# Kernel tuning notes

Measured on AMD Instinct MI355X. Metric: run time of the kernel, lower is better.

Reference implementation:

```python
import math
import jax, jax.numpy as jnp
import numpy as np

N_EMBD = 1024
N_HEAD = 16
EPS = 1e-5


def get_alibi_slopes(n_head):
    def pow2_slopes(n):
        start = 2 ** (-2 ** (-(math.log2(n) - 3)))
        return [start * start ** i for i in range(n)]
    if math.log2(n_head).is_integer():
        slopes = pow2_slopes(n_head)
    else:
        c = 2 ** math.floor(math.log2(n_head))
        slopes = pow2_slopes(c)
        extra = pow2_slopes(2 * c)[0::2]
        slopes.extend(extra[: n_head - c])
    return jnp.asarray(slopes, dtype=jnp.float32)


def layernorm(x, w, b):
    mu = jnp.mean(x, axis=-1, keepdims=True)
    var = jnp.var(x, axis=-1, keepdims=True)
    return (x - mu) * jax.lax.rsqrt(var + EPS) * w + b


def setup_inputs() -> dict:
    key = jax.random.key(0)
    ks = jax.random.split(key, 8)
    C = N_EMBD
    B, T = 2, 2048
    s = 0.02
    return {
        "x": jax.random.normal(ks[0], (B, T, C), dtype=jnp.float32),
        "ln1_w": jnp.ones((C,), jnp.float32),
        "ln1_b": jnp.zeros((C,), jnp.float32),
        "w_qkv": jax.random.normal(ks[1], (C, 3 * C), dtype=jnp.float32) * s,
        "b_qkv": jnp.zeros((3 * C,), jnp.float32),
        "w_proj": jax.random.normal(ks[2], (C, C), dtype=jnp.float32) * s,
        "b_proj": jnp.zeros((C,), jnp.float32),
        "ln2_w": jnp.ones((C,), jnp.float32),
        "ln2_b": jnp.zeros((C,), jnp.float32),
        "w_fc": jax.random.normal(ks[3], (C, 4 * C), dtype=jnp.float32) * s,
        "b_fc": jnp.zeros((4 * C,), jnp.float32),
        "w_fc2": jax.random.normal(ks[4], (4 * C, C), dtype=jnp.float32) * s,
        "b_fc2": jnp.zeros((C,), jnp.float32),
    }


def reference(x, ln1_w, ln1_b, w_qkv, b_qkv, w_proj, b_proj,
              ln2_w, ln2_b, w_fc, b_fc, w_fc2, b_fc2):
    B, T, C = x.shape
    H = N_HEAD
    D = C // H

    # --- attention with ALiBi ---
    h = layernorm(x, ln1_w, ln1_b)
    qkv = h @ w_qkv + b_qkv                       # [B,T,3C]
    q, k, v = jnp.split(qkv, 3, axis=-1)
    q = q.reshape(B, T, H, D).transpose(0, 2, 1, 3)  # [B,H,T,D]
    k = k.reshape(B, T, H, D).transpose(0, 2, 1, 3)
    v = v.reshape(B, T, H, D).transpose(0, 2, 1, 3)

    att = jnp.einsum('bhqd,bhkd->bhqk', q, k) * (1.0 / math.sqrt(D))

    pos = jnp.arange(T, dtype=jnp.float32)
    distances = pos[:, None] - pos[None, :]        # [T,T], i-j
    slopes = get_alibi_slopes(H)[:, None, None]     # [H,1,1]
    bias = slopes * distances[None, :, :]           # [H,T,T]
    causal = jnp.triu(jnp.ones((T, T), dtype=bool), k=1)
    bias = jnp.where(causal[None, :, :], -jnp.inf, bias)

    att = jax.nn.softmax(att + bias[None], axis=-1)
    y = jnp.einsum('bhqk,bhkd->bhqd', att, v)
    y = y.transpose(0, 2, 1, 3).reshape(B, T, C)
    x = x + y @ w_proj + b_proj

    # --- MLP ---
    h = layernorm(x, ln2_w, ln2_b)
    h = jax.nn.gelu(h @ w_fc + b_fc, approximate=False)
    x = x + h @ w_fc2 + b_fc2
    return x
```

## Files before the change

### kernel.cpp

```cpp
#include <hip/hip_runtime.h>
#include <hip/hip_bf16.h>
#include <math.h>

#define N_EMBD 1024
#define N_HEADC 16
#define HEAD_D 64

typedef __attribute__((ext_vector_type(8))) short short8;
typedef __attribute__((ext_vector_type(4))) float floatx4;

__device__ __forceinline__ ushort f2b(float f) {
    __hip_bfloat16 h = __float2bfloat16(f);
    return *reinterpret_cast<ushort*>(&h);
}

__device__ __forceinline__ void async_cp16(const void* gsrc, void* ldst) {
    __builtin_amdgcn_global_load_lds(
        (const __attribute__((address_space(1))) void*)gsrc,
        (__attribute__((address_space(3))) void*)ldst, 16, 0, 0);
}

__device__ __forceinline__ int xcd_swizzle(int bid, int nwg) {
    const int q = nwg >> 3, r = nwg & 7;
    const int xcd = bid & 7, loc = bid >> 3;
    return (xcd < r ? xcd * (q + 1) : r * (q + 1) + (xcd - r) * q) + loc;
}

template <int CTRL>
__device__ __forceinline__ float dppf(float x) {
    int r = __builtin_amdgcn_update_dpp(0, __builtin_bit_cast(int, x),
                                        CTRL, 0xF, 0xF, true);
    return __builtin_bit_cast(float, r);
}
__device__ __forceinline__ float redmax16(float x) {
    x = fmaxf(x, dppf<0xB1>(x));
    x = fmaxf(x, dppf<0x4E>(x));
    x = fmaxf(x, dppf<0x141>(x));
    x = fmaxf(x, dppf<0x140>(x));
    return x;
}
__device__ __forceinline__ float redsum16(float x) {
    x += dppf<0xB1>(x);
    x += dppf<0x4E>(x);
    x += dppf<0x141>(x);
    x += dppf<0x140>(x);
    return x;
}

__global__ __launch_bounds__(256) void ln_kernel(const float* __restrict__ x,
                                                 const float* __restrict__ w,
                                                 const float* __restrict__ b,
                                                 ushort* __restrict__ out) {
    const int row = blockIdx.x;
    const int t = threadIdx.x;
    const float4 v = reinterpret_cast<const float4*>(x + (size_t)row * N_EMBD)[t];
    float s  = v.x + v.y + v.z + v.w;
    float ss = v.x * v.x + v.y * v.y + v.z * v.z + v.w * v.w;
    for (int o = 32; o > 0; o >>= 1) {
        s  += __shfl_down(s, o);
        ss += __shfl_down(ss, o);
    }
    __shared__ float as_[4], ass_[4];
    const int wid = t >> 6, lane = t & 63;
    if (lane == 0) { as_[wid] = s; ass_[wid] = ss; }
    __syncthreads();
    const float ts  = as_[0] + as_[1] + as_[2] + as_[3];
    const float tss = ass_[0] + ass_[1] + ass_[2] + ass_[3];
    const float mu  = ts * (1.f / N_EMBD);
    const float var = tss * (1.f / N_EMBD) - mu * mu;
    const float inv = rsqrtf(var + 1e-5f);
    const float4 wv = reinterpret_cast<const float4*>(w)[t];
    const float4 bv = reinterpret_cast<const float4*>(b)[t];
    ushort4 o;
    o.x = f2b((v.x - mu) * inv * wv.x + bv.x);
    o.y = f2b((v.y - mu) * inv * wv.y + bv.y);
    o.z = f2b((v.z - mu) * inv * wv.z + bv.z);
    o.w = f2b((v.w - mu) * inv * wv.w + bv.w);
    reinterpret_cast<ushort4*>(out + (size_t)row * N_EMBD)[t] = o;
}

__global__ void convtrans_kernel(const float* __restrict__ W,
                                 ushort* __restrict__ Wt, int K, int N) {
    __shared__ float tile[32][33];
    const int tid = threadIdx.x;
    const int r = tid >> 3;
    const int c4 = (tid & 7) * 4;
    const int bx = blockIdx.x, by = blockIdx.y;

    float4 v = *(const float4*)&W[((size_t)(by * 32 + r)) * N + bx * 32 + c4];
    tile[r][c4 + 0] = v.x; tile[r][c4 + 1] = v.y;
    tile[r][c4 + 2] = v.z; tile[r][c4 + 3] = v.w;
    __syncthreads();

    ushort4 u;
    u.x = f2b(tile[c4 + 0][r]); u.y = f2b(tile[c4 + 1][r]);
    u.z = f2b(tile[c4 + 2][r]); u.w = f2b(tile[c4 + 3][r]);
    *(ushort4*)&Wt[((size_t)(bx * 32 + r)) * K + by * 32 + c4] = u;
}

__device__ __forceinline__ void gemm_stage(
        const ushort* __restrict__ A, const ushort* __restrict__ Bt,
        ushort* As, ushort* Bs,
        int m0, int n0, int K, int k0, int w, int lane) {
#pragma unroll
    for (int l = 0; l < 2; l++) {
        const int cbase = w * 128 + l * 64;
        const int c = cbase + lane;
        const int row = c >> 2, kc8 = (c & 3) * 8;
        async_cp16(A  + (size_t)(m0 + row) * K + k0 + kc8, &As[cbase * 8]);
        async_cp16(Bt + (size_t)(n0 + row) * K + k0 + kc8, &Bs[cbase * 8]);
    }
}

__device__ __forceinline__ void gemm_compute(
        const ushort* As, const ushort* Bs, floatx4 (*acc)[4],
        int wm, int wn, int quad, int l16) {
    short8 a[4], bf[4];
#pragma unroll
    for (int i = 0; i < 4; i++)
        a[i] = *(const short8*)&As[(wm * 64 + i * 16 + l16) * 32 + quad * 8];
#pragma unroll
    for (int j = 0; j < 4; j++)
        bf[j] = *(const short8*)&Bs[(wn * 64 + j * 16 + l16) * 32 + quad * 8];
#pragma unroll
    for (int i = 0; i < 4; i++)
#pragma unroll
        for (int j = 0; j < 4; j++)
            acc[i][j] = __builtin_amdgcn_mfma_f32_16x16x32_bf16(
                a[i], bf[j], acc[i][j], 0, 0, 0);
}

__global__ __launch_bounds__(256) void gemm_bf16_kernel(
        const ushort* __restrict__ A,
        const ushort* __restrict__ Bt,
        const float* __restrict__ bias,
        const float* __restrict__ residual,
        float* __restrict__ out32,
        ushort* __restrict__ out16,
        int M, int N, int K, int do_gelu) {
    __shared__ ushort As[2][128 * 32];
    __shared__ ushort Bs[2][128 * 32];

    const int tid  = threadIdx.x;
    const int w    = tid >> 6;
    const int lane = tid & 63;
    const int quad = lane >> 4;
    const int l16  = lane & 15;
    const int wm   = w >> 1;
    const int wn   = w & 1;

    int bid = blockIdx.y * gridDim.x + blockIdx.x;
    bid = xcd_swizzle(bid, gridDim.x * gridDim.y);
    const int bx = bid % gridDim.x;
    const int by = bid / gridDim.x;
    const int m0 = by * 128;
    const int n0 = bx * 128;

    const int kchunk = K / gridDim.z;
    const int kbeg   = blockIdx.z * kchunk;
    if (gridDim.z > 1)
        out32 += (size_t)blockIdx.z * M * N;

    floatx4 acc[4][4];
#pragma unroll
    for (int i = 0; i < 4; i++)
#pragma unroll
        for (int j = 0; j < 4; j++) acc[i][j] = (floatx4){0.f, 0.f, 0.f, 0.f};

    const int nt = kchunk >> 5;

    gemm_stage(A, Bt, As[0], Bs[0], m0, n0, K, kbeg, w, lane);
    __syncthreads();

    for (int t = 0; t < nt; t += 2) {
        gemm_stage(A, Bt, As[1], Bs[1], m0, n0, K, kbeg + ((t + 1) << 5), w, lane);
        gemm_compute(As[0], Bs[0], acc, wm, wn, quad, l16);
        __syncthreads();
        if (t + 2 < nt)
            gemm_stage(A, Bt, As[0], Bs[0], m0, n0, K, kbeg + ((t + 2) << 5), w, lane);
        gemm_compute(As[1], Bs[1], acc, wm, wn, quad, l16);
        __syncthreads();
    }

#pragma unroll
    for (int i = 0; i < 4; i++) {
#pragma unroll
        for (int j = 0; j < 4; j++) {
            const int nn = n0 + wn * 64 + j * 16 + l16;
            const float bv = bias ? bias[nn] : 0.f;
#pragma unroll
            for (int r = 0; r < 4; r++) {
                const int mm = m0 + wm * 64 + i * 16 + quad * 4 + r;
                float v = acc[i][j][r] + bv;
                if (do_gelu) v = 0.5f * v * (1.f + erff(v * 0.70710678118654752f));
                if (residual) v += residual[(size_t)mm * N + nn];
                if (out32) out32[(size_t)mm * N + nn] = v;
                if (out16) out16[(size_t)mm * N + nn] = f2b(v);
            }
        }
    }
}

__global__ __launch_bounds__(256) void combine_kernel(
        const float* __restrict__ p0, const float* __restrict__ p1,
        const float* __restrict__ bias, float* __restrict__ out) {
    const int i = blockIdx.x * 256 + threadIdx.x;
    const float4 a = ((const float4*)p0)[i];
    const float4 c = ((const float4*)p1)[i];
    const float4 bb = ((const float4*)bias)[i & 255];
    float4 o = ((float4*)out)[i];
    o.x += a.x + c.x + bb.x;
    o.y += a.y + c.y + bb.y;
    o.z += a.z + c.z + bb.z;
    o.w += a.w + c.w + bb.w;
    ((float4*)out)[i] = o;
}

#define AT_PAD 72
#define LOG2E 1.4426950408889634f

__device__ __forceinline__ void attn_tile_step(
        short8 aq0, short8 aq1,
        ushort (*__restrict__ Ks)[AT_PAD],
        ushort (*__restrict__ Vt)[AT_PAD],
        ushort (*__restrict__ Ps)[AT_PAD],
        float* m_r, float* l_r, floatx4* acc,
        int q0, int kt, bool domask,
        float qs2, float slope2, const float* skb,
        int w, int quad, int l16) {
    floatx4 sfrag[4];
#pragma unroll
    for (int kb = 0; kb < 4; kb++) {
        const int kcol = kb * 16 + l16;
        short8 bk0 = *(const short8*)&Ks[kcol][quad * 8];
        short8 bk1 = *(const short8*)&Ks[kcol][32 + quad * 8];
        floatx4 s = (floatx4){0.f, 0.f, 0.f, 0.f};
        s = __builtin_amdgcn_mfma_f32_16x16x32_bf16(aq0, bk0, s, 0, 0, 0);
        s = __builtin_amdgcn_mfma_f32_16x16x32_bf16(aq1, bk1, s, 0, 0, 0);
        sfrag[kb] = s;
    }

    const int psw = ((w * 4 + quad) & 7) << 3;
    int pcol[4];
#pragma unroll
    for (int kb = 0; kb < 4; kb++) pcol[kb] = (kb * 16 + l16) ^ psw;

    const float ktb = (float)(kt * 64);
#pragma unroll
    for (int r = 0; r < 4; r++) {
        const int q = q0 + w * 16 + quad * 4 + r;
        const float rowc = slope2 * ((float)q - ktb);
        float sv[4];
        float rm = -INFINITY;
#pragma unroll
        for (int kb = 0; kb < 4; kb++) {
            float s = fmaf(sfrag[kb][r], qs2, rowc) - skb[kb];
            if (domask) {
                const int k = kt * 64 + kb * 16 + l16;
                s = (k <= q) ? s : -INFINITY;
            }
            sv[kb] = s;
            rm = fmaxf(rm, s);
        }
        rm = redmax16(rm);
        if (rm > m_r[r]) {
            const float corr = exp2f(m_r[r] - rm);
            m_r[r] = rm;
            l_r[r] *= corr;
#pragma unroll
            for (int db = 0; db < 4; db++) acc[db][r] *= corr;
        }
        float rs = 0.f;
#pragma unroll
        for (int kb = 0; kb < 4; kb++) {
            const float pv = exp2f(sv[kb] - m_r[r]);
            rs += pv;
            Ps[w * 16 + quad * 4 + r][pcol[kb]] = f2b(pv);
        }
        rs = redsum16(rs);
        l_r[r] += rs;
    }

    const int prw = ((w * 4 + (l16 >> 2)) & 7) << 3;
    short8 ap0 = *(const short8*)&Ps[w * 16 + l16][(quad * 8) ^ prw];
    short8 ap1 = *(const short8*)&Ps[w * 16 + l16][(32 + quad * 8) ^ prw];
#pragma unroll
    for (int db = 0; db < 4; db++) {
        const int dv = db * 16 + l16;
        const int svw = ((db * 4 + (l16 >> 2)) & 7) << 3;
        short8 bv0 = *(const short8*)&Vt[dv][(quad * 8) ^ svw];
        short8 bv1 = *(const short8*)&Vt[dv][(32 + quad * 8) ^ svw];
        acc[db] = __builtin_amdgcn_mfma_f32_16x16x32_bf16(ap0, bv0, acc[db], 0, 0, 0);
        acc[db] = __builtin_amdgcn_mfma_f32_16x16x32_bf16(ap1, bv1, acc[db], 0, 0, 0);
    }
}

__global__ __launch_bounds__(256) void attn_mfma_kernel(
        const ushort* __restrict__ qkv, ushort* __restrict__ y,
        float* __restrict__ opart, float* __restrict__ mpart,
        float* __restrict__ lpart, int B, int T) {
    const int C3 = 3 * N_EMBD;

    const int lin = xcd_swizzle(blockIdx.x, gridDim.x);
    const int bh = lin / 48;
    const int s  = lin % 48;
    int qt, cc, ktb_i, kte;
    bool split;
    if (s < 32) {
        split = true;
        qt = 31 - (s >> 1);
        cc = s & 1;
        const int hc = (qt + 2) >> 1;
        ktb_i = cc ? hc : 0;
        kte   = cc ? qt : hc - 1;
    } else {
        split = false;
        qt = 47 - s;
        cc = 0;
        ktb_i = 0;
        kte = qt;
    }
    const int b = bh >> 4, h = bh & 15;

    const int tid  = threadIdx.x;
    const int lane = tid & 63;
    const int w    = tid >> 6;
    const int quad = lane >> 4;
    const int l16  = lane & 15;

    __shared__ ushort QPs[64][AT_PAD];
    __shared__ ushort Ks[64][AT_PAD];
    __shared__ ushort Vt[64][AT_PAD];

    const float slope  = exp2f(-0.5f * (float)(h + 1));
    const float slope2 = slope * LOG2E;
    const float qs2    = 0.125f * LOG2E;
    float skb[4];
#pragma unroll
    for (int kb = 0; kb < 4; kb++) skb[kb] = slope2 * (float)(kb * 16 + l16);

    const int q0 = qt * 64;
    const size_t hb = (size_t)b * T * C3 + (size_t)h * HEAD_D;

    int srow[4], sd0[4], svr[4];
#pragma unroll
    for (int i = 0; i < 4; i++) {
        const int idx = tid + i * 256;
        srow[i] = idx >> 4;
        sd0[i]  = (idx & 15) * 4;
        svr[i]  = srow[i] ^ ((idx & 7) << 3);
    }

#pragma unroll
    for (int i = 0; i < 4; i++) {
        *(ushort4*)&QPs[srow[i]][sd0[i]] =
            *(const ushort4*)&qkv[hb + (size_t)(q0 + srow[i]) * C3 + sd0[i]];
    }
    __syncthreads();

    const int mrow = w * 16 + l16;
    short8 aq0 = *(const short8*)&QPs[mrow][quad * 8];
    short8 aq1 = *(const short8*)&QPs[mrow][32 + quad * 8];

    float m_r[4], l_r[4];
    floatx4 acc[4];
#pragma unroll
    for (int r = 0; r < 4; r++) {
        m_r[r] = -INFINITY; l_r[r] = 0.f;
        acc[r] = (floatx4){0.f, 0.f, 0.f, 0.f};
    }

#pragma unroll
    for (int i = 0; i < 4; i++) {
        const size_t src = hb + (size_t)(ktb_i * 64 + srow[i]) * C3 + sd0[i];
        *(ushort4*)&Ks[srow[i]][sd0[i]] = *(const ushort4*)&qkv[src + N_EMBD];
        ushort4 vv = *(const ushort4*)&qkv[src + 2 * N_EMBD];
        Vt[sd0[i] + 0][svr[i]] = vv.x;
        Vt[sd0[i] + 1][svr[i]] = vv.y;
        Vt[sd0[i] + 2][svr[i]] = vv.z;
        Vt[sd0[i] + 3][svr[i]] = vv.w;
    }
    __syncthreads();

    for (int kt = ktb_i; kt <= kte; kt++) {
        ushort4 kreg[4], vreg[4];
        const bool pf = (kt < kte);
        if (pf) {
#pragma unroll
            for (int i = 0; i < 4; i++) {
                const size_t src =
                    hb + (size_t)((kt + 1) * 64 + srow[i]) * C3 + sd0[i];
                kreg[i] = *(const ushort4*)&qkv[src + N_EMBD];
                vreg[i] = *(const ushort4*)&qkv[src + 2 * N_EMBD];
            }
        }

        attn_tile_step(aq0, aq1, Ks, Vt, QPs, m_r, l_r, acc,
                       q0, kt, kt == qt, qs2, slope2, skb, w, quad, l16);
        __syncthreads();

        if (pf) {
#pragma unroll
            for (int i = 0; i < 4; i++) {
                *(ushort4*)&Ks[srow[i]][sd0[i]] = kreg[i];
                Vt[sd0[i] + 0][svr[i]] = vreg[i].x;
                Vt[sd0[i] + 1][svr[i]] = vreg[i].y;
                Vt[sd0[i] + 2][svr[i]] = vreg[i].z;
                Vt[sd0[i] + 3][svr[i]] = vreg[i].w;
            }
        }
        __syncthreads();
    }

    if (!split) {
#pragma unroll
        for (int r = 0; r < 4; r++) {
            const int qa = q0 + w * 16 + quad * 4 + r;
            const float ia = 1.f / l_r[r];
#pragma unroll
            for (int db = 0; db < 4; db++) {
                y[((size_t)b * T + qa) * N_EMBD + h * HEAD_D + db * 16 + l16] =
                    f2b(acc[db][r] * ia);
            }
        }
    } else {
        const int pidx = (bh * 16 + (qt - 16)) * 2 + cc;
#pragma unroll
        for (int r = 0; r < 4; r++) {
            const int row = w * 16 + quad * 4 + r;
#pragma unroll
            for (int db = 0; db < 4; db++) {
                opart[((size_t)pidx * 64 + row) * 64 + db * 16 + l16] =
                    acc[db][r];
            }
            if (l16 == 0) {
                mpart[pidx * 64 + row] = m_r[r];
                lpart[pidx * 64 + row] = l_r[r];
            }
        }
    }
}

__global__ __launch_bounds__(256) void attn_combine_kernel(
        const float* __restrict__ opart, const float* __restrict__ mpart,
        const float* __restrict__ lpart, ushort* __restrict__ y, int T) {
    const int x  = blockIdx.x;
    const int bh = x >> 4;
    const int qt = 16 + (x & 15);
    const int b  = bh >> 4, h = bh & 15;
    const int t  = threadIdx.x;
    const int row = t >> 2;
    const int dq  = (t & 3) << 4;
    const int p0 = x * 2, p1 = p0 + 1;

    const float m0 = mpart[p0 * 64 + row], m1 = mpart[p1 * 64 + row];
    const float l0 = lpart[p0 * 64 + row], l1 = lpart[p1 * 64 + row];
    const float M  = fmaxf(m0, m1);
    const float w0 = exp2f(m0 - M), w1 = exp2f(m1 - M);
    const float inv = 1.f / (l0 * w0 + l1 * w1);

    const float* o0 = &opart[((size_t)p0 * 64 + row) * 64 + dq];
    const float* o1 = &opart[((size_t)p1 * 64 + row) * 64 + dq];
    ushort* yr = &y[((size_t)b * T + qt * 64 + row) * N_EMBD + h * HEAD_D + dq];
#pragma unroll
    for (int j = 0; j < 16; j += 4) {
        const float4 a = *(const float4*)&o0[j];
        const float4 c = *(const float4*)&o1[j];
        yr[j + 0] = f2b((a.x * w0 + c.x * w1) * inv);
        yr[j + 1] = f2b((a.y * w0 + c.y * w1) * inv);
        yr[j + 2] = f2b((a.z * w0 + c.z * w1) * inv);
        yr[j + 3] = f2b((a.w * w0 + c.w * w1) * inv);
    }
}

extern "C" void kernel_launch(void* const* d_in, const int* in_sizes, int n_in,
                              void* d_out, int out_size, void* d_ws, size_t ws_size,
                              hipStream_t stream) {
    const int B = 2, T = 2048, C = N_EMBD;
    const int M = B * T;

    const float* x      = (const float*)d_in[0];
    const float* ln1_w  = (const float*)d_in[1];
    const float* ln1_b  = (const float*)d_in[2];
    const float* w_qkv  = (const float*)d_in[3];
    const float* b_qkv  = (const float*)d_in[4];
    const float* w_proj = (const float*)d_in[5];
    const float* b_proj = (const float*)d_in[6];
    const float* ln2_w  = (const float*)d_in[7];
    const float* ln2_b  = (const float*)d_in[8];
    const float* w_fc   = (const float*)d_in[9];
    const float* b_fc   = (const float*)d_in[10];
    const float* w_fc2  = (const float*)d_in[11];
    const float* b_fc2  = (const float*)d_in[12];
    float* out = (float*)d_out;

    char* ws = (char*)d_ws;
    size_t off = 0;
    ushort* wt_qkv  = (ushort*)(ws + off); off += (size_t)3 * C * C * 2;
    ushort* wt_proj = (ushort*)(ws + off); off += (size_t)C * C * 2;
    ushort* wt_fc   = (ushort*)(ws + off); off += (size_t)4 * C * C * 2;
    ushort* wt_fc2  = (ushort*)(ws + off); off += (size_t)4 * C * C * 2;
    ushort* h16     = (ushort*)(ws + off); off += (size_t)M * C * 2;
    ushort* qkv16   = (ushort*)(ws + off); off += (size_t)M * 3 * C * 2;
    ushort* y16     = (ushort*)(ws + off); off += (size_t)M * C * 2;
    ushort* fc16    = (ushort*)(ws + off); off += (size_t)M * 4 * C * 2;

    convtrans_kernel<<<dim3(3 * C / 32, C / 32), 256, 0, stream>>>(w_qkv, wt_qkv, C, 3 * C);
    convtrans_kernel<<<dim3(C / 32, C / 32), 256, 0, stream>>>(w_proj, wt_proj, C, C);
    convtrans_kernel<<<dim3(4 * C / 32, C / 32), 256, 0, stream>>>(w_fc, wt_fc, C, 4 * C);
    convtrans_kernel<<<dim3(C / 32, 4 * C / 32), 256, 0, stream>>>(w_fc2, wt_fc2, 4 * C, C);

    ln_kernel<<<M, 256, 0, stream>>>(x, ln1_w, ln1_b, h16);

    gemm_bf16_kernel<<<dim3(3 * C / 128, M / 128), 256, 0, stream>>>(
        h16, wt_qkv, b_qkv, nullptr, nullptr, qkv16, M, 3 * C, C, 0);

    float* aop = (float*)fc16;
    float* amp = aop + (size_t)1024 * 64 * 64;
    float* alp = amp + (size_t)1024 * 64;
    attn_mfma_kernel<<<32 * 48, 256, 0, stream>>>(
        qkv16, y16, aop, amp, alp, B, T);
    attn_combine_kernel<<<512, 256, 0, stream>>>(aop, amp, alp, y16, T);

    gemm_bf16_kernel<<<dim3(C / 128, M / 128), 256, 0, stream>>>(
        y16, wt_proj, b_proj, x, out, nullptr, M, C, C, 0);

    ln_kernel<<<M, 256, 0, stream>>>(out, ln2_w, ln2_b, h16);

    gemm_bf16_kernel<<<dim3(4 * C / 128, M / 128), 256, 0, stream>>>(
        h16, wt_fc, b_fc, nullptr, nullptr, fc16, M, 4 * C, C, 1);

    float* part = (float*)h16;
    gemm_bf16_kernel<<<dim3(C / 128, M / 128, 2), 256, 0, stream>>>(
        fc16, wt_fc2, nullptr, nullptr, part, nullptr, M, C, 4 * C, 0);
    combine_kernel<<<(M * C) / (256 * 4), 256, 0, stream>>>(
        part, part + (size_t)M * C, b_fc2, out);
}
```

Before: 437.0 us.

## Compute transposed S tile so each lane owns one query row in attention

Swaps the MFMA operands in the QK^T step so the score fragment is S^T: each lane now holds 16 scores for a single query row instead of 4 rows. Row max and sum then need only two cross-lane shuffles per tile instead of a DPP reduction per row, and each lane keeps one m/l scalar. P is written to LDS as packed ushort4 without the XOR swizzle. The cost is extra shuffles to broadcast the rescale factors to accumulator rows, and possible LDS bank conflicts on the unswizzled P writes and reads.

```diff
diff --git a/kernel.cpp b/kernel.cpp
--- a/kernel.cpp
+++ b/kernel.cpp
@@ -24,27 +24,6 @@
     const int q = nwg >> 3, r = nwg & 7;
     const int xcd = bid & 7, loc = bid >> 3;
     return (xcd < r ? xcd * (q + 1) : r * (q + 1) + (xcd - r) * q) + loc;
-}
-
-template <int CTRL>
-__device__ __forceinline__ float dppf(float x) {
-    int r = __builtin_amdgcn_update_dpp(0, __builtin_bit_cast(int, x),
-                                        CTRL, 0xF, 0xF, true);
-    return __builtin_bit_cast(float, r);
-}
-__device__ __forceinline__ float redmax16(float x) {
-    x = fmaxf(x, dppf<0xB1>(x));
-    x = fmaxf(x, dppf<0x4E>(x));
-    x = fmaxf(x, dppf<0x141>(x));
-    x = fmaxf(x, dppf<0x140>(x));
-    return x;
-}
-__device__ __forceinline__ float redsum16(float x) {
-    x += dppf<0xB1>(x);
-    x += dppf<0x4E>(x);
-    x += dppf<0x141>(x);
-    x += dppf<0x140>(x);
-    return x;
 }
 
 __global__ __launch_bounds__(256) void ln_kernel(const float* __restrict__ x,
@@ -224,66 +203,75 @@
         ushort (*__restrict__ Ks)[AT_PAD],
         ushort (*__restrict__ Vt)[AT_PAD],
         ushort (*__restrict__ Ps)[AT_PAD],
-        float* m_r, float* l_r, floatx4* acc,
-        int q0, int kt, bool domask,
-        float qs2, float slope2, const float* skb,
-        int w, int quad, int l16) {
+        float& m_row, float& l_row, floatx4* acc,
+        int qrow, int kt, bool domask,
+        float qs2, float alibi_q, float skb16, const float* skq4,
+        int w, int quad, int l16, int lane) {
     floatx4 sfrag[4];
 #pragma unroll
     for (int kb = 0; kb < 4; kb++) {
-        const int kcol = kb * 16 + l16;
-        short8 bk0 = *(const short8*)&Ks[kcol][quad * 8];
-        short8 bk1 = *(const short8*)&Ks[kcol][32 + quad * 8];
+        const int krow = kb * 16 + l16;
+        short8 ak0 = *(const short8*)&Ks[krow][quad * 8];
+        short8 ak1 = *(const short8*)&Ks[krow][32 + quad * 8];
         floatx4 s = (floatx4){0.f, 0.f, 0.f, 0.f};
-        s = __builtin_amdgcn_mfma_f32_16x16x32_bf16(aq0, bk0, s, 0, 0, 0);
-        s = __builtin_amdgcn_mfma_f32_16x16x32_bf16(aq1, bk1, s, 0, 0, 0);
+        s = __builtin_amdgcn_mfma_f32_16x16x32_bf16(ak0, aq0, s, 0, 0, 0);
+        s = __builtin_amdgcn_mfma_f32_16x16x32_bf16(ak1, aq1, s, 0, 0, 0);
         sfrag[kb] = s;
     }
 
-    const int psw = ((w * 4 + quad) & 7) << 3;
-    int pcol[4];
-#pragma unroll
-    for (int kb = 0; kb < 4; kb++) pcol[kb] = (kb * 16 + l16) ^ psw;
-
-    const float ktb = (float)(kt * 64);
-#pragma unroll
-    for (int r = 0; r < 4; r++) {
-        const int q = q0 + w * 16 + quad * 4 + r;
-        const float rowc = slope2 * ((float)q - ktb);
-        float sv[4];
-        float rm = -INFINITY;
-#pragma unroll
-        for (int kb = 0; kb < 4; kb++) {
-            float s = fmaf(sfrag[kb][r], qs2, rowc) - skb[kb];
+    const float rowc = alibi_q - skb16 * (float)(kt * 4);
+    float sv[4][4];
+    float rm = -INFINITY;
+#pragma unroll
+    for (int kb = 0; kb < 4; kb++) {
+        const float rck = rowc - skb16 * (float)kb;
+#pragma unroll
+        for (int r = 0; r < 4; r++) {
+            float s = fmaf(sfrag[kb][r], qs2, rck - skq4[r]);
             if (domask) {
-                const int k = kt * 64 + kb * 16 + l16;
-                s = (k <= q) ? s : -INFINITY;
+                const int k = kt * 64 + kb * 16 + quad * 4 + r;
+                s = (k <= qrow) ? s : -INFINITY;
             }
-            sv[kb] = s;
+            sv[kb][r] = s;
             rm = fmaxf(rm, s);
         }
-        rm = redmax16(rm);
-        if (rm > m_r[r]) {
-            const float corr = exp2f(m_r[r] - rm);
-            m_r[r] = rm;
-            l_r[r] *= corr;
-#pragma unroll
-            for (int db = 0; db < 4; db++) acc[db][r] *= corr;
-        }
-        float rs = 0.f;
-#pragma unroll
-        for (int kb = 0; kb < 4; kb++) {
-            const float pv = exp2f(sv[kb] - m_r[r]);
-            rs += pv;
-            Ps[w * 16 + quad * 4 + r][pcol[kb]] = f2b(pv);
-        }
-        rs = redsum16(rs);
-        l_r[r] += rs;
-    }
-
-    const int prw = ((w * 4 + (l16 >> 2)) & 7) << 3;
-    short8 ap0 = *(const short8*)&Ps[w * 16 + l16][(quad * 8) ^ prw];
-    short8 ap1 = *(const short8*)&Ps[w * 16 + l16][(32 + quad * 8) ^ prw];
+    }
+    rm = fmaxf(rm, __shfl_xor(rm, 16));
+    rm = fmaxf(rm, __shfl_xor(rm, 32));
+
+    if (__any(rm > m_row)) {
+        const float mn = fmaxf(rm, m_row);
+        const float corr = exp2f(m_row - mn);
+        m_row = mn;
+        l_row *= corr;
+        float cr[4];
+#pragma unroll
+        for (int r = 0; r < 4; r++)
+            cr[r] = __shfl(corr, (lane & 48) + quad * 4 + r);
+#pragma unroll
+        for (int db = 0; db < 4; db++)
+#pragma unroll
+            for (int r = 0; r < 4; r++) acc[db][r] *= cr[r];
+    }
+
+    float rs = 0.f;
+#pragma unroll
+    for (int kb = 0; kb < 4; kb++) {
+        const float p0 = exp2f(sv[kb][0] - m_row);
+        const float p1 = exp2f(sv[kb][1] - m_row);
+        const float p2 = exp2f(sv[kb][2] - m_row);
+        const float p3 = exp2f(sv[kb][3] - m_row);
+        rs += (p0 + p1) + (p2 + p3);
+        ushort4 pw;
+        pw.x = f2b(p0); pw.y = f2b(p1); pw.z = f2b(p2); pw.w = f2b(p3);
+        *(ushort4*)&Ps[w * 16 + l16][kb * 16 + quad * 4] = pw;
+    }
+    rs += __shfl_xor(rs, 16);
+    rs += __shfl_xor(rs, 32);
+    l_row += rs;
+
+    short8 ap0 = *(const short8*)&Ps[w * 16 + l16][quad * 8];
+    short8 ap1 = *(const short8*)&Ps[w * 16 + l16][32 + quad * 8];
 #pragma unroll
     for (int db = 0; db < 4; db++) {
         const int dv = db * 16 + l16;
@@ -335,11 +323,15 @@
     const float slope  = exp2f(-0.5f * (float)(h + 1));
     const float slope2 = slope * LOG2E;
     const float qs2    = 0.125f * LOG2E;
-    float skb[4];
-#pragma unroll
-    for (int kb = 0; kb < 4; kb++) skb[kb] = slope2 * (float)(kb * 16 + l16);
 
     const int q0 = qt * 64;
+    const int qrow = q0 + w * 16 + l16;
+    const float alibi_q = slope2 * (float)qrow;
+    const float skb16   = slope2 * 16.f;
+    float skq4[4];
+#pragma unroll
+    for (int r = 0; r < 4; r++) skq4[r] = slope2 * (float)(quad * 4 + r);
+
     const size_t hb = (size_t)b * T * C3 + (size_t)h * HEAD_D;
 
     int srow[4], sd0[4], svr[4];
@@ -362,13 +354,10 @@
     short8 aq0 = *(const short8*)&QPs[mrow][quad * 8];
     short8 aq1 = *(const short8*)&QPs[mrow][32 + quad * 8];
 
-    float m_r[4], l_r[4];
+    float m_row = -INFINITY, l_row = 0.f;
     floatx4 acc[4];
 #pragma unroll
-    for (int r = 0; r < 4; r++) {
-        m_r[r] = -INFINITY; l_r[r] = 0.f;
-        acc[r] = (floatx4){0.f, 0.f, 0.f, 0.f};
-    }
+    for (int r = 0; r < 4; r++) acc[r] = (floatx4){0.f, 0.f, 0.f, 0.f};
 
 #pragma unroll
     for (int i = 0; i < 4; i++) {
@@ -395,8 +384,9 @@
             }
         }
 
-        attn_tile_step(aq0, aq1, Ks, Vt, QPs, m_r, l_r, acc,
-                       q0, kt, kt == qt, qs2, slope2, skb, w, quad, l16);
+        attn_tile_step(aq0, aq1, Ks, Vt, QPs, m_row, l_row, acc,
+                       qrow, kt, kt == qt, qs2, alibi_q, skb16, skq4,
+                       w, quad, l16, lane);
         __syncthreads();
 
         if (pf) {
@@ -413,14 +403,18 @@
     }
 
     if (!split) {
+        const float li = 1.f / l_row;
+        float ia[4];
+#pragma unroll
+        for (int r = 0; r < 4; r++)
+            ia[r] = __shfl(li, (lane & 48) + quad * 4 + r);
 #pragma unroll
         for (int r = 0; r < 4; r++) {
             const int qa = q0 + w * 16 + quad * 4 + r;
-            const float ia = 1.f / l_r[r];
 #pragma unroll
             for (int db = 0; db < 4; db++) {
                 y[((size_t)b * T + qa) * N_EMBD + h * HEAD_D + db * 16 + l16] =
-                    f2b(acc[db][r] * ia);
+                    f2b(acc[db][r] * ia[r]);
             }
         }
     } else {
@@ -433,10 +427,10 @@
                 opart[((size_t)pidx * 64 + row) * 64 + db * 16 + l16] =
                     acc[db][r];
             }
-            if (l16 == 0) {
-                mpart[pidx * 64 + row] = m_r[r];
-                lpart[pidx * 64 + row] = l_r[r];
-            }
+        }
+        if (quad == 0) {
+            mpart[pidx * 64 + w * 16 + l16] = m_row;
+            lpart[pidx * 64 + w * 16 + l16] = l_row;
         }
     }
 }
```

Result: faster. 423.1 us (-3.2%).
